# Performance work log

Hardware: AMD Instinct MI355X
Metric: run time of the kernel (lower is better)

Reference implementation:

```python
import jax, jax.numpy as jnp
import numpy as np

N = 2048      # oscillators
K = 8         # neighbors per oscillator (connectivity0)
B = 32        # batch
T = 20        # time_steps
EPS0 = 1.0    # update_rate
ANNEAL = 0.0  # anneal


def setup_inputs() -> dict:
    key = jax.random.key(0)
    k1, k2, k3 = jax.random.split(key, 3)
    coupling = jax.random.normal(k1, (B, N, K), dtype=jnp.float32)
    connectivity = jax.random.randint(k2, (N, K), 0, N)
    phase0 = 2.0 * jnp.pi * jax.random.uniform(k3, (B, N), dtype=jnp.float32)
    omega = jnp.zeros((B, N), dtype=jnp.float32)
    return {"coupling": coupling, "phase0": phase0, "omega": omega,
            "connectivity": connectivity}


def reference(coupling, phase0, omega, connectivity):
    # Scatter sparse per-neighbor couplings [B,N,K] into dense [B,N,N]
    # (torch scatter_ dim=2 with the same index per batch element).
    rows = jnp.arange(N)[:, None]                      # [N,1]
    C = jnp.zeros((B, N, N), coupling.dtype).at[:, rows, connectivity].set(coupling)
    # n = number of nonzero couplings per row  [B,N]
    n = jnp.abs(jnp.sign(C)).sum(axis=2)

    def step(carry, i):
        phase, eps = carry                             # phase [B,N]
        s, c = jnp.sin(phase), jnp.cos(phase)
        Cs = jnp.einsum('bnm,bm->bn', C, s)
        Cc = jnp.einsum('bnm,bm->bn', C, c)
        delta = eps * (Cs * c - Cc * s) / n
        phase_new = phase + delta + omega
        # eps_anneal called after each update with step index i
        eps_new = eps - ANNEAL * i.astype(eps.dtype) * eps / T
        return (phase_new, eps_new), phase_new

    (_, _), phases = jax.lax.scan(step, (phase0, jnp.float32(EPS0)), jnp.arange(T))
    # phase_list: initial phase followed by T updated phases  [T+1,B,N]
    return jnp.concatenate([phase0[None], phases], axis=0)
```

## Files before the change

kernel.cpp:

```cpp
#include <hip/hip_runtime.h>

#define NN 2048
#define KK 8
#define BB 32
#define TT 20

__global__ __launch_bounds__(1024) void osci_kernel(
    const float* __restrict__ coupling,
    const float* __restrict__ phase0,
    const float* __restrict__ omega,
    const int*   __restrict__ conn,
    float*       __restrict__ out)
{
    const int b   = blockIdx.x;
    const int tid = threadIdx.x;

    __shared__ float ph_buf[2 * NN];

    int   cidx[2][KK];
    float w[2][KK];
    float inv_n[2];
    float om[2];
    float ph[2];

    for (int t = 0; t < 2; ++t) {
        const int i = tid + t * 1024;
        float p = phase0[b * NN + i];
        ph[t] = p;
        ph_buf[i] = p;
        out[(size_t)b * NN + i] = p;
        om[t] = omega[b * NN + i];

        int   jj[KK];
        float vv[KK];
        #pragma unroll
        for (int k = 0; k < KK; ++k) {
            jj[k] = conn[i * KK + k];
            vv[k] = coupling[((size_t)b * NN + i) * KK + k];
        }
        int cnt = 0;
        #pragma unroll
        for (int k = 0; k < KK; ++k) {
            bool over = false;
            #pragma unroll
            for (int k2 = k + 1; k2 < KK; ++k2) over = over || (jj[k2] == jj[k]);
            if (over) vv[k] = 0.0f;
            if (vv[k] != 0.0f) ++cnt;
        }
        #pragma unroll
        for (int k = 0; k < KK; ++k) { cidx[t][k] = jj[k]; w[t][k] = vv[k]; }
        inv_n[t] = 1.0f / (float)cnt;
    }
    __syncthreads();

    float* outp = out + ((size_t)BB + b) * NN;

    #pragma unroll 1
    for (int sp = 0; sp < TT; sp += 2) {
        #pragma unroll
        for (int t = 0; t < 2; ++t) {
            const int i = tid + t * 1024;
            float acc = 0.0f;
            #pragma unroll
            for (int k = 0; k < KK; ++k) {
                const float pj = ph_buf[cidx[t][k]];
                acc += w[t][k] * __sinf(pj - ph[t]);
            }
            const float pn = ph[t] + acc * inv_n[t] + om[t];
            ph[t] = pn;
            ph_buf[NN + i] = pn;
            outp[i] = pn;
        }
        asm volatile("s_waitcnt lgkmcnt(0)" ::: "memory");
        __builtin_amdgcn_s_barrier();
        asm volatile("" ::: "memory");
        outp += (size_t)BB * NN;

        #pragma unroll
        for (int t = 0; t < 2; ++t) {
            const int i = tid + t * 1024;
            float acc = 0.0f;
            #pragma unroll
            for (int k = 0; k < KK; ++k) {
                const float pj = ph_buf[NN + cidx[t][k]];
                acc += w[t][k] * __sinf(pj - ph[t]);
            }
            const float pn = ph[t] + acc * inv_n[t] + om[t];
            ph[t] = pn;
            ph_buf[i] = pn;
            outp[i] = pn;
        }
        asm volatile("s_waitcnt lgkmcnt(0)" ::: "memory");
        __builtin_amdgcn_s_barrier();
        asm volatile("" ::: "memory");
        outp += (size_t)BB * NN;
    }
}

extern "C" void kernel_launch(void* const* d_in, const int* in_sizes, int n_in,
                              void* d_out, int out_size, void* d_ws, size_t ws_size,
                              hipStream_t stream) {
    const float* coupling = (const float*)d_in[0];
    const float* phase0   = (const float*)d_in[1];
    const float* omega    = (const float*)d_in[2];
    const int*   conn     = (const int*)d_in[3];
    float* out = (float*)d_out;

    osci_kernel<<<BB, 1024, 0, stream>>>(coupling, phase0, omega, conn, out);
}
```

Measured before the change: 79.69 us.

## Mix sin-difference and precomputed sincos table paths across the two oscillator halves

The first half of each thread's oscillators keeps computing sin(pj - pi) per neighbor. The second half switches to reading precomputed (sin, cos) pairs from a new shared float2 table and uses the expanded identity Cs*c - Cc*s. Each step therefore computes two sincos per thread instead of eight sines for that half. It also vectorizes the initial connectivity and coupling loads with int4/float4. The cost is extra LDS traffic and storage for the sincos table, plus extra writes per step. This balances the transcendental (SFU) load against LDS bandwidth.

```diff
diff --git a/kernel.cpp b/kernel.cpp
--- a/kernel.cpp
+++ b/kernel.cpp
@@ -15,29 +15,35 @@
     const int b   = blockIdx.x;
     const int tid = threadIdx.x;
 
-    __shared__ float ph_buf[2 * NN];
+    __shared__ float  ph_tab[2 * NN];
+    __shared__ float2 sc_tab[2 * NN];
 
     int   cidx[2][KK];
     float w[2][KK];
     float inv_n[2];
     float om[2];
     float ph[2];
+    float si1, ci1;
 
     for (int t = 0; t < 2; ++t) {
         const int i = tid + t * 1024;
         float p = phase0[b * NN + i];
         ph[t] = p;
-        ph_buf[i] = p;
+        float s, c;
+        __sincosf(p, &s, &c);
+        if (t == 1) { si1 = s; ci1 = c; }
+        ph_tab[i] = p;
+        sc_tab[i] = make_float2(s, c);
         out[(size_t)b * NN + i] = p;
         om[t] = omega[b * NN + i];
 
-        int   jj[KK];
-        float vv[KK];
-        #pragma unroll
-        for (int k = 0; k < KK; ++k) {
-            jj[k] = conn[i * KK + k];
-            vv[k] = coupling[((size_t)b * NN + i) * KK + k];
-        }
+        const int4*   c4 = (const int4*)  &conn[i * KK];
+        const float4* w4 = (const float4*)&coupling[((size_t)b * NN + i) * KK];
+        int4   ja = c4[0], jb = c4[1];
+        float4 va = w4[0], vb = w4[1];
+        int   jj[KK] = { ja.x, ja.y, ja.z, ja.w, jb.x, jb.y, jb.z, jb.w };
+        float vv[KK] = { va.x, va.y, va.z, va.w, vb.x, vb.y, vb.z, vb.w };
+
         int cnt = 0;
         #pragma unroll
         for (int k = 0; k < KK; ++k) {
@@ -57,38 +63,68 @@
 
     #pragma unroll 1
     for (int sp = 0; sp < TT; sp += 2) {
-        #pragma unroll
-        for (int t = 0; t < 2; ++t) {
-            const int i = tid + t * 1024;
+        {
+            const float p0 = ph[0];
             float acc = 0.0f;
             #pragma unroll
             for (int k = 0; k < KK; ++k) {
-                const float pj = ph_buf[cidx[t][k]];
-                acc += w[t][k] * __sinf(pj - ph[t]);
+                acc += w[0][k] * __sinf(ph_tab[cidx[0][k]] - p0);
             }
-            const float pn = ph[t] + acc * inv_n[t] + om[t];
-            ph[t] = pn;
-            ph_buf[NN + i] = pn;
-            outp[i] = pn;
+            const float pn0 = p0 + acc * inv_n[0] + om[0];
+
+            float cs = 0.0f, cc = 0.0f;
+            #pragma unroll
+            for (int k = 0; k < KK; ++k) {
+                const float2 v = sc_tab[cidx[1][k]];
+                cs += w[1][k] * v.x;
+                cc += w[1][k] * v.y;
+            }
+            const float pn1 = ph[1] + (cs * ci1 - cc * si1) * inv_n[1] + om[1];
+
+            ph[0] = pn0; ph[1] = pn1;
+            float s0, c0;
+            __sincosf(pn0, &s0, &c0);
+            __sincosf(pn1, &si1, &ci1);
+            ph_tab[NN + tid]        = pn0;
+            ph_tab[NN + tid + 1024] = pn1;
+            sc_tab[NN + tid]        = make_float2(s0, c0);
+            sc_tab[NN + tid + 1024] = make_float2(si1, ci1);
+            outp[tid]        = pn0;
+            outp[tid + 1024] = pn1;
         }
         asm volatile("s_waitcnt lgkmcnt(0)" ::: "memory");
         __builtin_amdgcn_s_barrier();
         asm volatile("" ::: "memory");
         outp += (size_t)BB * NN;
 
-        #pragma unroll
-        for (int t = 0; t < 2; ++t) {
-            const int i = tid + t * 1024;
+        {
+            const float p0 = ph[0];
             float acc = 0.0f;
             #pragma unroll
             for (int k = 0; k < KK; ++k) {
-                const float pj = ph_buf[NN + cidx[t][k]];
-                acc += w[t][k] * __sinf(pj - ph[t]);
+                acc += w[0][k] * __sinf(ph_tab[NN + cidx[0][k]] - p0);
             }
-            const float pn = ph[t] + acc * inv_n[t] + om[t];
-            ph[t] = pn;
-            ph_buf[i] = pn;
-            outp[i] = pn;
+            const float pn0 = p0 + acc * inv_n[0] + om[0];
+
+            float cs = 0.0f, cc = 0.0f;
+            #pragma unroll
+            for (int k = 0; k < KK; ++k) {
+                const float2 v = sc_tab[NN + cidx[1][k]];
+                cs += w[1][k] * v.x;
+                cc += w[1][k] * v.y;
+            }
+            const float pn1 = ph[1] + (cs * ci1 - cc * si1) * inv_n[1] + om[1];
+
+            ph[0] = pn0; ph[1] = pn1;
+            float s0, c0;
+            __sincosf(pn0, &s0, &c0);
+            __sincosf(pn1, &si1, &ci1);
+            ph_tab[tid]        = pn0;
+            ph_tab[tid + 1024] = pn1;
+            sc_tab[tid]        = make_float2(s0, c0);
+            sc_tab[tid + 1024] = make_float2(si1, ci1);
+            outp[tid]        = pn0;
+            outp[tid + 1024] = pn1;
         }
         asm volatile("s_waitcnt lgkmcnt(0)" ::: "memory");
         __builtin_amdgcn_s_barrier();
```

Result: slower. 81.74 us (+2.6%).

## Halve block size, give each thread four oscillators, batch LDS gathers, vectorize loads

Applied to the files above, without the earlier changes.

Drops the block from 1024 to 512 threads, so each thread now owns four oscillators instead of two. Each step first issues all 32 neighbor phase gathers from shared memory, then computes the sines, which exposes more memory-level parallelism per thread. The per-oscillator connectivity and coupling loads during setup become int4/float4 vector loads. The cost is higher register pressure and fewer waves for the barrier-bound loop, with only 32 blocks running on the GPU.

```diff
diff --git a/kernel.cpp b/kernel.cpp
--- a/kernel.cpp
+++ b/kernel.cpp
@@ -4,8 +4,10 @@
 #define KK 8
 #define BB 32
 #define TT 20
+#define NT 512
+#define OPT (NN / NT)
 
-__global__ __launch_bounds__(1024) void osci_kernel(
+__global__ __launch_bounds__(NT) void osci_kernel(
     const float* __restrict__ coupling,
     const float* __restrict__ phase0,
     const float* __restrict__ omega,
@@ -15,29 +17,29 @@
     const int b   = blockIdx.x;
     const int tid = threadIdx.x;
 
-    __shared__ float ph_buf[2 * NN];
+    __shared__ float ph_tab[2 * NN];
 
-    int   cidx[2][KK];
-    float w[2][KK];
-    float inv_n[2];
-    float om[2];
-    float ph[2];
+    int   cidx[OPT][KK];
+    float w[OPT][KK];
+    float inv_n[OPT];
+    float om[OPT];
+    float ph[OPT];
 
-    for (int t = 0; t < 2; ++t) {
-        const int i = tid + t * 1024;
+    for (int t = 0; t < OPT; ++t) {
+        const int i = tid + t * NT;
         float p = phase0[b * NN + i];
         ph[t] = p;
-        ph_buf[i] = p;
+        ph_tab[i] = p;
         out[(size_t)b * NN + i] = p;
         om[t] = omega[b * NN + i];
 
-        int   jj[KK];
-        float vv[KK];
-        #pragma unroll
-        for (int k = 0; k < KK; ++k) {
-            jj[k] = conn[i * KK + k];
-            vv[k] = coupling[((size_t)b * NN + i) * KK + k];
-        }
+        const int4*   c4 = (const int4*)  &conn[i * KK];
+        const float4* w4 = (const float4*)&coupling[((size_t)b * NN + i) * KK];
+        int4   ja = c4[0], jb = c4[1];
+        float4 va = w4[0], vb = w4[1];
+        int   jj[KK] = { ja.x, ja.y, ja.z, ja.w, jb.x, jb.y, jb.z, jb.w };
+        float vv[KK] = { va.x, va.y, va.z, va.w, vb.x, vb.y, vb.z, vb.w };
+
         int cnt = 0;
         #pragma unroll
         for (int k = 0; k < KK; ++k) {
@@ -57,38 +59,52 @@
 
     #pragma unroll 1
     for (int sp = 0; sp < TT; sp += 2) {
-        #pragma unroll
-        for (int t = 0; t < 2; ++t) {
-            const int i = tid + t * 1024;
-            float acc = 0.0f;
+        {
+            float pj[OPT][KK];
             #pragma unroll
-            for (int k = 0; k < KK; ++k) {
-                const float pj = ph_buf[cidx[t][k]];
-                acc += w[t][k] * __sinf(pj - ph[t]);
+            for (int t = 0; t < OPT; ++t)
+                #pragma unroll
+                for (int k = 0; k < KK; ++k)
+                    pj[t][k] = ph_tab[cidx[t][k]];
+
+            #pragma unroll
+            for (int t = 0; t < OPT; ++t) {
+                const int i = tid + t * NT;
+                float acc = 0.0f;
+                #pragma unroll
+                for (int k = 0; k < KK; ++k)
+                    acc += w[t][k] * __sinf(pj[t][k] - ph[t]);
+                const float pn = ph[t] + acc * inv_n[t] + om[t];
+                ph[t] = pn;
+                ph_tab[NN + i] = pn;
+                outp[i] = pn;
             }
-            const float pn = ph[t] + acc * inv_n[t] + om[t];
-            ph[t] = pn;
-            ph_buf[NN + i] = pn;
-            outp[i] = pn;
         }
         asm volatile("s_waitcnt lgkmcnt(0)" ::: "memory");
         __builtin_amdgcn_s_barrier();
         asm volatile("" ::: "memory");
         outp += (size_t)BB * NN;
 
-        #pragma unroll
-        for (int t = 0; t < 2; ++t) {
-            const int i = tid + t * 1024;
-            float acc = 0.0f;
+        {
+            float pj[OPT][KK];
             #pragma unroll
-            for (int k = 0; k < KK; ++k) {
-                const float pj = ph_buf[NN + cidx[t][k]];
-                acc += w[t][k] * __sinf(pj - ph[t]);
+            for (int t = 0; t < OPT; ++t)
+                #pragma unroll
+                for (int k = 0; k < KK; ++k)
+                    pj[t][k] = ph_tab[NN + cidx[t][k]];
+
+            #pragma unroll
+            for (int t = 0; t < OPT; ++t) {
+                const int i = tid + t * NT;
+                float acc = 0.0f;
+                #pragma unroll
+                for (int k = 0; k < KK; ++k)
+                    acc += w[t][k] * __sinf(pj[t][k] - ph[t]);
+                const float pn = ph[t] + acc * inv_n[t] + om[t];
+                ph[t] = pn;
+                ph_tab[i] = pn;
+                outp[i] = pn;
             }
-            const float pn = ph[t] + acc * inv_n[t] + om[t];
-            ph[t] = pn;
-            ph_buf[i] = pn;
-            outp[i] = pn;
         }
         asm volatile("s_waitcnt lgkmcnt(0)" ::: "memory");
         __builtin_amdgcn_s_barrier();
@@ -106,5 +122,5 @@
     const int*   conn     = (const int*)d_in[3];
     float* out = (float*)d_out;
 
-    osci_kernel<<<BB, 1024, 0, stream>>>(coupling, phase0, omega, conn, out);
+    osci_kernel<<<BB, NT, 0, stream>>>(coupling, phase0, omega, conn, out);
 }
```

New measurement: 85.41 us. 7.2% more time.
